# Optimization experiments

Hardware: AMD Instinct MI355X
Metric: run time of the kernel (lower is better)

## Reference

```python
import jax, jax.numpy as jnp
import numpy as np

EPS = 1e-8

def setup_inputs() -> dict:
    key = jax.random.key(0)
    k1, k2 = jax.random.split(key)
    B, IN, OUT, G = 32768, 256, 256, 5
    x = jax.random.normal(k1, (B, IN), dtype=jnp.float32)
    grid = jnp.linspace(-1.0, 1.0, G).astype(jnp.float32)
    coef = jax.random.normal(k2, (OUT, IN, G), dtype=jnp.float32) * 0.1
    scale = jnp.ones((OUT, IN), dtype=jnp.float32)
    bias = jnp.zeros((OUT,), dtype=jnp.float32)
    return {"x": x, "grid": grid, "coef": coef, "scale": scale, "bias": bias}

def reference(x, grid, coef, scale, bias):
    # global min-max normalization to [-1, 1]
    xmin, xmax = x.min(), x.max()
    xn = 2.0 * (x - xmin) / (xmax - xmin + EPS) - 1.0
    # cubic bump B-spline-like basis: (batch, in, grid)
    dist = jnp.abs(xn[..., None] - grid)
    basis = jnp.where(dist < 1.0, 1.0 - dist ** 3, 0.0)
    basis = basis / (basis.sum(axis=-1, keepdims=True) + EPS)
    # fused contraction over (in, grid); equals ((basis*coef).sum(-1)*scale).sum(-1)
    w = coef * scale[..., None]          # (out, in, grid)
    out = jnp.einsum('big,oig->bo', basis, w) + bias
    return out
```

## Files before the change

### kernel.cpp

```cpp
#include <hip/hip_runtime.h>
#include <stdint.h>


#define B_SZ   32768
#define IN_SZ  256
#define OUT_SZ 256
#define EPSF   1e-8f
#define NMB    2048

typedef __bf16 bf16x8 __attribute__((ext_vector_type(8)));
typedef unsigned short ushort8 __attribute__((ext_vector_type(8)));
typedef float floatx16 __attribute__((ext_vector_type(16)));

union frag_u { uint4 u; bf16x8 v; };

__device__ __forceinline__ unsigned short f2bf(float f) {
  unsigned u = __float_as_uint(f);
  u += 0x7FFFu + ((u >> 16) & 1u);
  return (unsigned short)(u >> 16);
}


__global__ void __launch_bounds__(256) prep_kernel(const float* __restrict__ coef,
                                                   const float* __restrict__ scale,
                                                   const float* __restrict__ x,
                                                   unsigned short* __restrict__ wf,
                                                   float* __restrict__ part, int n4) {
  const int t = threadIdx.x;
  if (blockIdx.x < 256) {
    int idx = blockIdx.x * 256 + t;
    int o = idx >> 8, i = idx & 255;
    float s = scale[idx];
    const float* c = coef + (size_t)idx * 5;
    ushort8 v;
    v[0] = f2bf(c[0] * s); v[1] = f2bf(c[1] * s); v[2] = f2bf(c[2] * s);
    v[3] = f2bf(c[3] * s); v[4] = f2bf(c[4] * s);
    v[5] = 0; v[6] = 0; v[7] = 0;
    int chunk = (((o >> 5) * 64 + (i >> 2)) * 2 + ((i >> 1) & 1)) * 64
                + (i & 1) * 32 + (o & 31);
    *(ushort8*)(wf + (size_t)chunk * 8) = v;
  } else {
    int mb = blockIdx.x - 256;
    const float4* x4 = (const float4*)x;
    int i = mb * 256 + t;
    float lmin = 1e30f, lmax = -1e30f;
    #pragma unroll
    for (int k = 0; k < 4; ++k) {
      float4 v = x4[i + k * (NMB * 256)];
      lmin = fminf(lmin, fminf(fminf(v.x, v.y), fminf(v.z, v.w)));
      lmax = fmaxf(lmax, fmaxf(fmaxf(v.x, v.y), fmaxf(v.z, v.w)));
    }
    #pragma unroll
    for (int off = 32; off >= 1; off >>= 1) {
      lmin = fminf(lmin, __shfl_down(lmin, off, 64));
      lmax = fmaxf(lmax, __shfl_down(lmax, off, 64));
    }
    __shared__ float smn[4], smx[4];
    if ((t & 63) == 0) { smn[t >> 6] = lmin; smx[t >> 6] = lmax; }
    __syncthreads();
    if (t == 0) {
      part[2 * mb]     = fminf(fminf(smn[0], smn[1]), fminf(smn[2], smn[3]));
      part[2 * mb + 1] = fmaxf(fmaxf(smx[0], smx[1]), fmaxf(smx[2], smx[3]));
    }
  }
}

__device__ __forceinline__ bf16x8 basisfrag(float xval, float scA, float scB) {
  float xn = fmaf(xval, scA, scB);
  float d0 = xn + 1.0f, d1 = xn + 0.5f, d3 = xn - 0.5f, d4 = xn - 1.0f;
  float b0 = fmaxf(fmaf(d0 * d0, -fabsf(d0), 1.0f), 0.0f);
  float b1 = fmaxf(fmaf(d1 * d1, -fabsf(d1), 1.0f), 0.0f);
  float b2 = fmaxf(fmaf(xn * xn, -fabsf(xn), 1.0f), 0.0f);
  float b3 = fmaxf(fmaf(d3 * d3, -fabsf(d3), 1.0f), 0.0f);
  float b4 = fmaxf(fmaf(d4 * d4, -fabsf(d4), 1.0f), 0.0f);
  float sum = ((b0 + b1) + (b2 + b3)) + b4;
  float inv = __builtin_amdgcn_rcpf(sum);
  b0 *= inv; b1 *= inv; b2 *= inv; b3 *= inv; b4 *= inv;
  frag_u r;
  r.u.x = __builtin_amdgcn_perm(__float_as_uint(b1), __float_as_uint(b0), 0x07060302u);
  r.u.y = __builtin_amdgcn_perm(__float_as_uint(b3), __float_as_uint(b2), 0x07060302u);
  r.u.z = __float_as_uint(b4) >> 16;
  r.u.w = 0u;
  return r.v;
}

__global__ void __launch_bounds__(256, 4) kan_gemm(
    const float* __restrict__ x,
    const unsigned short* __restrict__ wf,
    const float* __restrict__ bias,
    const float* __restrict__ part,
    float* __restrict__ out)
{
  __shared__ __align__(16) unsigned short Bb[2][8192];
  __shared__ float2 red[4];

  const int t = threadIdx.x;
  const int lane = t & 63;
  const int wm = t >> 6;
  const int sm = wm & 1;
  const int h  = wm >> 1;
  const int l31 = lane & 31, lh = lane >> 5;
  const int bRow = blockIdx.x * 64;
  const int bCol = blockIdx.y * 128;
  const int row = bRow + sm * 32 + l31;

  auto stage = [&](int c, int buf) {
    #pragma unroll
    for (int r = 0; r < 4; ++r) {
      int seg = r * 4 + wm;
      int sh = seg >> 3, sks = (seg >> 2) & 1, sot = seg & 3;
      const unsigned short* src = wf +
          ((size_t)(((blockIdx.y * 4 + sot) * 64 + (sh * 32 + c)) * 2 + sks)) * 512
          + (size_t)lane * 8;
      __builtin_amdgcn_global_load_lds(
          (const __attribute__((address_space(1))) unsigned int*)src,
          (__attribute__((address_space(3))) unsigned int*)(&Bb[buf][seg * 512 + lane * 8]),
          16, 0, 0);
    }
  };

  const float* xrow = x + (size_t)row * IN_SZ + h * 128;

  float4 xq = *(const float4*)(xrow);
  stage(0, 0);

  float mn = 1e30f, mx = -1e30f;
  const float2* part2 = (const float2*)part;
  #pragma unroll
  for (int k = 0; k < NMB / 256; ++k) {
    float2 p = part2[k * 256 + t];
    mn = fminf(mn, p.x); mx = fmaxf(mx, p.y);
  }
  #pragma unroll
  for (int off = 32; off >= 1; off >>= 1) {
    mn = fminf(mn, __shfl_down(mn, off, 64));
    mx = fmaxf(mx, __shfl_down(mx, off, 64));
  }
  if (lane == 0) red[wm] = make_float2(mn, mx);
  __syncthreads();
  mn = fminf(fminf(red[0].x, red[1].x), fminf(red[2].x, red[3].x));
  mx = fmaxf(fmaxf(red[0].y, red[1].y), fmaxf(red[2].y, red[3].y));
  const float scA = 2.0f / (mx - mn + EPSF);
  const float scB = -mn * scA - 1.0f;

  floatx16 acc[4] = {};
  bf16x8 bf[8];

  for (int c = 0; c < 32; ++c) {
    const int buf = c & 1;
    float4 xn;

    if (c < 31) {
      xn = *(const float4*)(xrow + (c + 1) * 4);
      stage(c + 1, buf ^ 1);
    }
    __builtin_amdgcn_sched_barrier(0);
    if (c < 31) asm volatile("s_waitcnt vmcnt(5)");
    else        asm volatile("s_waitcnt vmcnt(0)");
    __builtin_amdgcn_s_barrier();
    __builtin_amdgcn_sched_barrier(0);

    #pragma unroll
    for (int q = 0; q < 8; ++q) {
      int ni = q >> 1, ks = q & 1;
      bf[q] = *(const bf16x8*)(&Bb[buf][(h * 8 + ks * 4 + ni) * 512 + lane * 8]);
    }

    float xv0 = lh ? xq.y : xq.x;
    float xv1 = lh ? xq.w : xq.z;
    bf16x8 a0 = basisfrag(xv0, scA, scB);
    bf16x8 a1 = basisfrag(xv1, scA, scB);

    __builtin_amdgcn_s_setprio(1);
    #pragma unroll
    for (int ni = 0; ni < 4; ++ni) {
      acc[ni] = __builtin_amdgcn_mfma_f32_32x32x16_bf16(a0, bf[ni * 2 + 0], acc[ni], 0, 0, 0);
      acc[ni] = __builtin_amdgcn_mfma_f32_32x32x16_bf16(a1, bf[ni * 2 + 1], acc[ni], 0, 0, 0);
    }
    __builtin_amdgcn_s_setprio(0);

    if (c < 31) {
      xq = xn;
      __builtin_amdgcn_sched_barrier(0);
      __builtin_amdgcn_s_barrier();
      __builtin_amdgcn_sched_barrier(0);
    }
  }

  __syncthreads();
  float* Cb = (float*)Bb;
  {
    int eo = h ? 0 : 2;
    int e  = h ? 0 : 1;
    float* base = Cb + (sm * 2 + e) * 2048;
    #pragma unroll
    for (int ni2 = 0; ni2 < 2; ++ni2) {
      #pragma unroll
      for (int reg = 0; reg < 16; ++reg) {
        int r = 4 * lh + (reg & 3) + 8 * (reg >> 2);
        base[r * 64 + ni2 * 32 + l31] = acc[eo + ni2][reg];
      }
    }
  }
  __syncthreads();
  {
    int ko = h ? 2 : 0;
    const float* base = Cb + (sm * 2 + h) * 2048;
    #pragma unroll
    for (int ni2 = 0; ni2 < 2; ++ni2) {
      int o = bCol + h * 64 + ni2 * 32 + l31;
      float bs = bias[o];
      #pragma unroll
      for (int reg = 0; reg < 16; ++reg) {
        int r = 4 * lh + (reg & 3) + 8 * (reg >> 2);
        float v = acc[ko + ni2][reg] + base[r * 64 + ni2 * 32 + l31] + bs;
        out[(size_t)(bRow + sm * 32 + r) * OUT_SZ + o] = v;
      }
    }
  }
}

extern "C" void kernel_launch(void* const* d_in, const int* in_sizes, int n_in,
                              void* d_out, int out_size, void* d_ws, size_t ws_size,
                              hipStream_t stream) {
  const float* x     = (const float*)d_in[0];
  const float* coef  = (const float*)d_in[2];
  const float* scale = (const float*)d_in[3];
  const float* bias  = (const float*)d_in[4];
  float* out = (float*)d_out;

  size_t need = 16384 + (size_t)OUT_SZ * IN_SZ * 8 * 2;
  if (ws_size < need) return;

  float* part = (float*)d_ws;
  unsigned short* wf = (unsigned short*)((char*)d_ws + 16384);

  prep_kernel<<<256 + NMB, 256, 0, stream>>>(coef, scale, x, wf, part,
                                             (B_SZ * IN_SZ) / 4);
  dim3 g(B_SZ / 64, OUT_SZ / 128);
  kan_gemm<<<g, 256, 0, stream>>>(x, wf, bias, part, out);
}
```

Baseline: 140.4 us.

## Double the row tile per block so each B fragment feeds two MFMA row groups

```diff
diff --git a/kernel.cpp b/kernel.cpp
--- a/kernel.cpp
+++ b/kernel.cpp
@@ -84,14 +84,14 @@
   return r.v;
 }
 
-__global__ void __launch_bounds__(256, 4) kan_gemm(
+__global__ void __launch_bounds__(256, 2) kan_gemm(
     const float* __restrict__ x,
     const unsigned short* __restrict__ wf,
     const float* __restrict__ bias,
     const float* __restrict__ part,
     float* __restrict__ out)
 {
-  __shared__ __align__(16) unsigned short Bb[2][8192];
+  __shared__ __align__(16) unsigned short Bb[2][16384];
   __shared__ float2 red[4];
 
   const int t = threadIdx.x;
@@ -100,29 +100,34 @@
   const int sm = wm & 1;
   const int h  = wm >> 1;
   const int l31 = lane & 31, lh = lane >> 5;
-  const int bRow = blockIdx.x * 64;
+  const int bRow = blockIdx.x * 128;
   const int bCol = blockIdx.y * 128;
-  const int row = bRow + sm * 32 + l31;
 
   auto stage = [&](int c, int buf) {
     #pragma unroll
-    for (int r = 0; r < 4; ++r) {
-      int seg = r * 4 + wm;
-      int sh = seg >> 3, sks = (seg >> 2) & 1, sot = seg & 3;
+    for (int r = 0; r < 8; ++r) {
+      int s = r * 4 + wm;
+      int sh = s >> 4, sktr = (s >> 3) & 1, sks = (s >> 2) & 1, sni = s & 3;
       const unsigned short* src = wf +
-          ((size_t)(((blockIdx.y * 4 + sot) * 64 + (sh * 32 + c)) * 2 + sks)) * 512
+          ((size_t)(((blockIdx.y * 4 + sni) * 64 + (sh * 32 + c * 2 + sktr)) * 2 + sks)) * 512
           + (size_t)lane * 8;
       __builtin_amdgcn_global_load_lds(
           (const __attribute__((address_space(1))) unsigned int*)src,
-          (__attribute__((address_space(3))) unsigned int*)(&Bb[buf][seg * 512 + lane * 8]),
+          (__attribute__((address_space(3))) unsigned int*)(&Bb[buf][s * 512 + lane * 8]),
           16, 0, 0);
     }
   };
 
-  const float* xrow = x + (size_t)row * IN_SZ + h * 128;
-
-  float4 xq = *(const float4*)(xrow);
+  const float* xrow0 = x + (size_t)(bRow + sm * 64 + l31) * IN_SZ + h * 128;
+  const float* xrow1 = xrow0 + 32 * IN_SZ;
+
   stage(0, 0);
+  float4 xq0[2], xq1[2], xqn0[2], xqn1[2];
+  #pragma unroll
+  for (int j = 0; j < 2; ++j) {
+    xq0[j] = *(const float4*)(xrow0 + j * 4);
+    xq1[j] = *(const float4*)(xrow1 + j * 4);
+  }
 
   float mn = 1e30f, mx = -1e30f;
   const float2* part2 = (const float2*)part;
@@ -143,44 +148,57 @@
   const float scA = 2.0f / (mx - mn + EPSF);
   const float scB = -mn * scA - 1.0f;
 
-  floatx16 acc[4] = {};
+  floatx16 acc0[4] = {}, acc1[4] = {};
   bf16x8 bf[8];
 
-  for (int c = 0; c < 32; ++c) {
+  for (int c = 0; c < 16; ++c) {
     const int buf = c & 1;
-    float4 xn;
-
-    if (c < 31) {
-      xn = *(const float4*)(xrow + (c + 1) * 4);
+
+    if (c < 15) {
+      #pragma unroll
+      for (int j = 0; j < 2; ++j) {
+        xqn0[j] = *(const float4*)(xrow0 + (c + 1) * 8 + j * 4);
+        xqn1[j] = *(const float4*)(xrow1 + (c + 1) * 8 + j * 4);
+      }
       stage(c + 1, buf ^ 1);
     }
     __builtin_amdgcn_sched_barrier(0);
-    if (c < 31) asm volatile("s_waitcnt vmcnt(5)");
+    if (c < 15) asm volatile("s_waitcnt vmcnt(12)");
     else        asm volatile("s_waitcnt vmcnt(0)");
     __builtin_amdgcn_s_barrier();
     __builtin_amdgcn_sched_barrier(0);
 
     #pragma unroll
-    for (int q = 0; q < 8; ++q) {
-      int ni = q >> 1, ks = q & 1;
-      bf[q] = *(const bf16x8*)(&Bb[buf][(h * 8 + ks * 4 + ni) * 512 + lane * 8]);
-    }
-
-    float xv0 = lh ? xq.y : xq.x;
-    float xv1 = lh ? xq.w : xq.z;
-    bf16x8 a0 = basisfrag(xv0, scA, scB);
-    bf16x8 a1 = basisfrag(xv1, scA, scB);
-
-    __builtin_amdgcn_s_setprio(1);
-    #pragma unroll
-    for (int ni = 0; ni < 4; ++ni) {
-      acc[ni] = __builtin_amdgcn_mfma_f32_32x32x16_bf16(a0, bf[ni * 2 + 0], acc[ni], 0, 0, 0);
-      acc[ni] = __builtin_amdgcn_mfma_f32_32x32x16_bf16(a1, bf[ni * 2 + 1], acc[ni], 0, 0, 0);
-    }
-    __builtin_amdgcn_s_setprio(0);
-
-    if (c < 31) {
-      xq = xn;
+    for (int ktr = 0; ktr < 2; ++ktr) {
+      #pragma unroll
+      for (int q = 0; q < 8; ++q)
+        bf[q] = *(const bf16x8*)(&Bb[buf][(h * 16 + ktr * 8 + q) * 512 + lane * 8]);
+
+      float4 q0 = xq0[ktr], q1 = xq1[ktr];
+      bf16x8 a00 = basisfrag(lh ? q0.y : q0.x, scA, scB);
+      bf16x8 a01 = basisfrag(lh ? q0.w : q0.z, scA, scB);
+      bf16x8 a10 = basisfrag(lh ? q1.y : q1.x, scA, scB);
+      bf16x8 a11 = basisfrag(lh ? q1.w : q1.z, scA, scB);
+
+      __builtin_amdgcn_s_setprio(1);
+      #pragma unroll
+      for (int ni = 0; ni < 4; ++ni) {
+        acc0[ni] = __builtin_amdgcn_mfma_f32_32x32x16_bf16(a00, bf[ni], acc0[ni], 0, 0, 0);
+        acc1[ni] = __builtin_amdgcn_mfma_f32_32x32x16_bf16(a10, bf[ni], acc1[ni], 0, 0, 0);
+      }
+      #pragma unroll
+      for (int ni = 0; ni < 4; ++ni) {
+        acc0[ni] = __builtin_amdgcn_mfma_f32_32x32x16_bf16(a01, bf[4 + ni], acc0[ni], 0, 0, 0);
+        acc1[ni] = __builtin_amdgcn_mfma_f32_32x32x16_bf16(a11, bf[4 + ni], acc1[ni], 0, 0, 0);
+      }
+      __builtin_amdgcn_s_setprio(0);
+    }
+
+    if (c < 15) {
+      #pragma unroll
+      for (int j = 0; j < 2; ++j) {
+        xq0[j] = xqn0[j]; xq1[j] = xqn1[j];
+      }
       __builtin_amdgcn_sched_barrier(0);
       __builtin_amdgcn_s_barrier();
       __builtin_amdgcn_sched_barrier(0);
@@ -192,20 +210,21 @@
   {
     int eo = h ? 0 : 2;
     int e  = h ? 0 : 1;
-    float* base = Cb + (sm * 2 + e) * 2048;
+    float* base = Cb + (sm * 2 + e) * 4096;
     #pragma unroll
     for (int ni2 = 0; ni2 < 2; ++ni2) {
       #pragma unroll
       for (int reg = 0; reg < 16; ++reg) {
         int r = 4 * lh + (reg & 3) + 8 * (reg >> 2);
-        base[r * 64 + ni2 * 32 + l31] = acc[eo + ni2][reg];
+        base[r * 64 + ni2 * 32 + l31]        = acc0[eo + ni2][reg];
+        base[(r + 32) * 64 + ni2 * 32 + l31] = acc1[eo + ni2][reg];
       }
     }
   }
   __syncthreads();
   {
     int ko = h ? 2 : 0;
-    const float* base = Cb + (sm * 2 + h) * 2048;
+    const float* base = Cb + (sm * 2 + h) * 4096;
     #pragma unroll
     for (int ni2 = 0; ni2 < 2; ++ni2) {
       int o = bCol + h * 64 + ni2 * 32 + l31;
@@ -213,8 +232,10 @@
       #pragma unroll
       for (int reg = 0; reg < 16; ++reg) {
         int r = 4 * lh + (reg & 3) + 8 * (reg >> 2);
-        float v = acc[ko + ni2][reg] + base[r * 64 + ni2 * 32 + l31] + bs;
-        out[(size_t)(bRow + sm * 32 + r) * OUT_SZ + o] = v;
+        float v0 = acc0[ko + ni2][reg] + base[r * 64 + ni2 * 32 + l31] + bs;
+        float v1 = acc1[ko + ni2][reg] + base[(r + 32) * 64 + ni2 * 32 + l31] + bs;
+        out[(size_t)(bRow + sm * 64 + r) * OUT_SZ + o] = v0;
+        out[(size_t)(bRow + sm * 64 + r + 32) * OUT_SZ + o] = v1;
       }
     }
   }
@@ -237,6 +258,6 @@
 
   prep_kernel<<<256 + NMB, 256, 0, stream>>>(coef, scale, x, wf, part,
                                              (B_SZ * IN_SZ) / 4);
-  dim3 g(B_SZ / 64, OUT_SZ / 128);
+  dim3 g(B_SZ / 128, OUT_SZ / 128);
   kan_gemm<<<g, 256, 0, stream>>>(x, wf, bias, part, out);
 }
```

Result: faster. 135.4 us (-3.5%).
